# Kernel optimization log

Measured on AMD Instinct MI355X. Metric: run time of the kernel, lower is better.

Reference implementation:

```python
import jax, jax.numpy as jnp
import numpy as np

N = 1_000_000
C = 128
NBINS = 15


def setup_inputs() -> dict:
    key = jax.random.key(0)
    k1, k2 = jax.random.split(key)
    logits = jax.random.normal(k1, (N, C), dtype=jnp.float32)
    labels = jax.random.randint(k2, (N,), 0, C, dtype=jnp.int64)
    return {"logits": logits, "labels": labels}


def reference(logits, labels):
    n = logits.shape[0]
    probs = jax.nn.softmax(logits, axis=1)
    confidences = jnp.max(probs, axis=1)                      # [N]
    predictions = jnp.argmax(probs, axis=1)                   # [N]
    accuracies = (predictions == labels).astype(jnp.float32)  # [N]

    # Equal-count (adaptive) bin edges: interp(linspace(0,N,nbins+1), arange(N), sort(conf))
    sorted_conf = jnp.sort(confidences)
    q = jnp.linspace(0.0, float(n), NBINS + 1)
    edges = jnp.interp(q, jnp.arange(n, dtype=jnp.float32), sorted_conf)  # [NBINS+1]

    # Bin i covers (edges[i], edges[i+1]] to match conf.gt(lower) & conf.le(upper).
    idx = jnp.searchsorted(edges[1:-1], confidences, side="left")  # [N] in [0, NBINS-1]
    valid = (confidences > edges[0]) & (confidences <= edges[-1])
    idx = jnp.where(valid, idx, NBINS)  # dump out-of-range into extra segment

    cnt = jax.ops.segment_sum(jnp.ones_like(confidences), idx, num_segments=NBINS + 1)[:NBINS]
    csum = jax.ops.segment_sum(confidences, idx, num_segments=NBINS + 1)[:NBINS]
    asum = jax.ops.segment_sum(accuracies, idx, num_segments=NBINS + 1)[:NBINS]

    prop = cnt / jnp.float32(n)
    safe = jnp.maximum(cnt, 1.0)
    gap = jnp.abs(csum / safe - asum / safe)
    ece = jnp.sum(jnp.where(cnt > 0, gap * prop, 0.0))
    return ece.reshape(1)
```

## Files before the change

### kernel.cpp

```cpp
#include <hip/hip_runtime.h>
#include <hip/hip_bf16.h>
#include <cstdint>

#define NROWS 1000000
#define NCLS  128
#define NBINS 15

#define FBASE 0x3B000000u
#define NB    73728
#define SCAN_T 1024
#define PER   (NB / SCAN_T)

#define OFF_CONF   0u
#define OFF_ACC    4000000u
#define OFF_HIST   5000000u
#define OFF_SUB    5294912u
#define OFF_BINS   5417792u
#define OFF_DONE   5418152u
#define OFF_TGTB   5418168u
#define OFF_TGTL   5418288u
#define OFF_EDGES  5418408u
#define ZERO_BYTES (OFF_TGTB - OFF_HIST)

#define ROW_BLOCKS 2048

__device__ __forceinline__ void reduce_row(float4 v0, float4 v1, int l16,
                                           float& c_out, int& mi_out)
{
    const int b0 = l16 * 4, b1 = 64 + l16 * 4;
    float m = v0.x; int mi = b0;
    if (v0.y > m) { m = v0.y; mi = b0 + 1; }
    if (v0.z > m) { m = v0.z; mi = b0 + 2; }
    if (v0.w > m) { m = v0.w; mi = b0 + 3; }
    if (v1.x > m) { m = v1.x; mi = b1; }
    if (v1.y > m) { m = v1.y; mi = b1 + 1; }
    if (v1.z > m) { m = v1.z; mi = b1 + 2; }
    if (v1.w > m) { m = v1.w; mi = b1 + 3; }
#pragma unroll
    for (int d = 1; d < 16; d <<= 1) {
        float om = __shfl_xor(m, d);
        int   oi = __shfl_xor(mi, d);
        if (om > m || (om == m && oi < mi)) { m = om; mi = oi; }
    }
    float s = __expf(v0.x - m) + __expf(v0.y - m) + __expf(v0.z - m) + __expf(v0.w - m)
            + __expf(v1.x - m) + __expf(v1.y - m) + __expf(v1.z - m) + __expf(v1.w - m);
#pragma unroll
    for (int d = 1; d < 16; d <<= 1) s += __shfl_xor(s, d);
    c_out  = 1.0f / s;
    mi_out = mi;
}

__device__ __forceinline__ int bucket_of(float c)
{
    int ub = (int)(__float_as_uint(c) - FBASE);
    int b  = ub >> 10;
    return b < 0 ? 0 : (b >= NB ? NB - 1 : b);
}

__global__ __launch_bounds__(256) void k_row(const float* __restrict__ logits,
                                             const int* __restrict__ labels,
                                             float* __restrict__ conf,
                                             unsigned char* __restrict__ acc,
                                             unsigned int* __restrict__ hist)
{
    const int g   = threadIdx.x >> 4;
    const int l16 = threadIdx.x & 15;
    const float4* lg4 = reinterpret_cast<const float4*>(logits);

    for (long long base = (long long)blockIdx.x * 32; base < NROWS;
         base += (long long)ROW_BLOCKS * 32) {
        const long long rowA = base + g * 2;

        const float4* p = lg4 + rowA * (NCLS / 4) + l16;
        const float4 a0 = p[0],  a1 = p[16];
        const float4 b0 = p[32], b1 = p[48];
        const int2 lab = *reinterpret_cast<const int2*>(labels + rowA);

        float cA, cB; int miA, miB;
        reduce_row(a0, a1, l16, cA, miA);
        reduce_row(b0, b1, l16, cB, miB);

        if (l16 == 0) {
            *reinterpret_cast<float2*>(conf + rowA) = make_float2(cA, cB);
            uchar2 a;
            a.x = (lab.x == miA) ? 1 : 0;
            a.y = (lab.y == miB) ? 1 : 0;
            *reinterpret_cast<uchar2*>(acc + rowA) = a;
            atomicAdd(&hist[bucket_of(cA)], 1u);
            atomicAdd(&hist[bucket_of(cB)], 1u);
        }
    }
}

__device__ __forceinline__ unsigned int rank_of(int s)
{
    if (s == 0)  return 0u;
    if (s == 29) return (unsigned int)(NROWS - 1);
    int i = (s + 1) >> 1;
    unsigned int k = (unsigned int)((long long)i * NROWS / 15);
    return k + ((s & 1) ? 0u : 1u);
}

__global__ __launch_bounds__(SCAN_T) void k_scan(const unsigned int* __restrict__ hist,
                                                 int* __restrict__ tgtb,
                                                 int* __restrict__ tgtl)
{
    __shared__ unsigned int v[SCAN_T];
    const int t = threadIdx.x;
    unsigned int s = 0;
    for (int j = 0; j < PER; j++) s += hist[t * PER + j];
    v[t] = s;
    __syncthreads();
    for (int off = 1; off < SCAN_T; off <<= 1) {
        unsigned int x = (t >= off) ? v[t - off] : 0u;
        __syncthreads();
        v[t] += x;
        __syncthreads();
    }
    const unsigned int run0 = v[t] - s;
    for (int s2 = 0; s2 < 30; s2++) {
        unsigned int r = rank_of(s2);
        if (r >= run0 && r < run0 + s) {
            unsigned int run = run0;
            for (int j = 0; j < PER; j++) {
                unsigned int c = hist[t * PER + j];
                if (r < run + c) { tgtb[s2] = t * PER + j; tgtl[s2] = (int)(r - run); break; }
                run += c;
            }
        }
    }
}

__global__ __launch_bounds__(256) void k_subhist(const float* __restrict__ conf,
                                                 const int* __restrict__ tgtb,
                                                 const int* __restrict__ tgtl,
                                                 unsigned int* __restrict__ sub,
                                                 float* __restrict__ edges,
                                                 unsigned int* __restrict__ done)
{
    __shared__ int tb[30];
    if (threadIdx.x < 30) tb[threadIdx.x] = tgtb[threadIdx.x];
    __syncthreads();
    const int stride = gridDim.x * blockDim.x;
    for (int i = blockIdx.x * blockDim.x + threadIdx.x; i < NROWS / 4; i += stride) {
        float4 c4 = reinterpret_cast<const float4*>(conf)[i];
        float cv[4] = {c4.x, c4.y, c4.z, c4.w};
#pragma unroll
        for (int e = 0; e < 4; e++) {
            int ub = (int)(__float_as_uint(cv[e]) - FBASE);
            int b  = ub >> 10;
            b = b < 0 ? 0 : (b >= NB ? NB - 1 : b);
            int lo = ub & 1023;
            for (int s = 0; s < 30; s++)
                if (b == tb[s]) atomicAdd(&sub[s * 1024 + lo], 1u);
        }
    }

    __syncthreads();
    __shared__ unsigned int isLast;
    if (threadIdx.x == 0) {
        __threadfence();
        isLast = (atomicAdd(done, 1u) == gridDim.x - 1) ? 1u : 0u;
    }
    __syncthreads();
    if (!isLast) return;
    __threadfence();

    __shared__ float val[32];
    const int k = threadIdx.x & 31;
    for (int slot = threadIdx.x >> 5; slot < 30; slot += 8) {
        const unsigned int local = (unsigned int)tgtl[slot];
        unsigned int cs[32];
        unsigned int csum = 0;
        const unsigned int* q = sub + slot * 1024 + k * 32;
#pragma unroll
        for (int j = 0; j < 32; j++) { cs[j] = q[j]; csum += cs[j]; }
        unsigned int incl = csum;
#pragma unroll
        for (int off = 1; off < 32; off <<= 1) {
            unsigned int x = __shfl_up(incl, off);
            if (k >= off) incl += x;
        }
        const unsigned int excl = incl - csum;
        if (local >= excl && local < excl + csum) {
            unsigned int run = excl;
            int subidx = 0;
#pragma unroll
            for (int j = 0; j < 32; j++) {
                if (local >= run && local < run + cs[j]) subidx = k * 32 + j;
                run += cs[j];
            }
            unsigned int bits = FBASE + ((unsigned int)tb[slot] << 10) + (unsigned int)subidx;
            val[slot] = __uint_as_float(bits);
        }
    }
    __syncthreads();
    if (threadIdx.x == 0) {
        edges[0]  = val[0];
        edges[15] = val[29];
        for (int i = 1; i <= 14; i++) {
            double q = (double)i * (double)NROWS / 15.0;
            long long kk = (long long)i * NROWS / 15;
            double f = q - (double)kk;
            edges[i] = (float)((1.0 - f) * (double)val[2 * i - 1] + f * (double)val[2 * i]);
        }
    }
}

__global__ __launch_bounds__(256) void k_bin(const float* __restrict__ conf,
                                             const unsigned char* __restrict__ acc,
                                             const float* __restrict__ edges,
                                             double* __restrict__ bins,
                                             unsigned int* __restrict__ done,
                                             float* __restrict__ out)
{
    __shared__ float se[16];
    __shared__ float lc[4][16], ls[4][16], la[4][16];
    const int w = threadIdx.x >> 6;
    if (threadIdx.x < 16) se[threadIdx.x] = edges[threadIdx.x];
    if (threadIdx.x < 64) {
        int a = threadIdx.x >> 4, b = threadIdx.x & 15;
        lc[a][b] = 0.f; ls[a][b] = 0.f; la[a][b] = 0.f;
    }
    __syncthreads();
    const int stride = gridDim.x * blockDim.x;
    for (int i = blockIdx.x * blockDim.x + threadIdx.x; i < NROWS / 4; i += stride) {
        float4 c4 = reinterpret_cast<const float4*>(conf)[i];
        uchar4 a4 = reinterpret_cast<const uchar4*>(acc)[i];
        float cv[4] = {c4.x, c4.y, c4.z, c4.w};
        unsigned char av[4] = {a4.x, a4.y, a4.z, a4.w};
#pragma unroll
        for (int e = 0; e < 4; e++) {
            float v = cv[e];
            if (v > se[0] && v <= se[15]) {
                int idx = 0;
#pragma unroll
                for (int j = 1; j <= 14; j++) idx += (se[j] < v) ? 1 : 0;
                atomicAdd(&lc[w][idx], 1.0f);
                atomicAdd(&ls[w][idx], v);
                atomicAdd(&la[w][idx], (float)av[e]);
            }
        }
    }
    __syncthreads();
    if (threadIdx.x < 15) {
        int t = threadIdx.x;
        atomicAdd(&bins[t],      (double)(lc[0][t] + lc[1][t] + lc[2][t] + lc[3][t]));
        atomicAdd(&bins[15 + t], (double)(ls[0][t] + ls[1][t] + ls[2][t] + ls[3][t]));
        atomicAdd(&bins[30 + t], (double)(la[0][t] + la[1][t] + la[2][t] + la[3][t]));
    }

    __syncthreads();
    __shared__ unsigned int isLast;
    if (threadIdx.x == 0) {
        __threadfence();
        isLast = (atomicAdd(done, 1u) == gridDim.x - 1) ? 1u : 0u;
    }
    __syncthreads();
    if (isLast && threadIdx.x == 0) {
        __threadfence();
        double ece = 0.0;
        for (int b = 0; b < NBINS; b++) {
            double cnt = bins[b];
            if (cnt > 0.0) {
                double safe = cnt < 1.0 ? 1.0 : cnt;
                double gap  = fabs(bins[15 + b] / safe - bins[30 + b] / safe);
                ece += gap * (cnt / (double)NROWS);
            }
        }
        out[0] = (float)ece;
    }
}

extern "C" void kernel_launch(void* const* d_in, const int* in_sizes, int n_in,
                              void* d_out, int out_size, void* d_ws, size_t ws_size,
                              hipStream_t stream)
{
    const float* logits = (const float*)d_in[0];
    const int*   labels = (const int*)d_in[1];
    char* ws = (char*)d_ws;

    float*         conf  = (float*)(ws + OFF_CONF);
    unsigned char* acc   = (unsigned char*)(ws + OFF_ACC);
    unsigned int*  hist  = (unsigned int*)(ws + OFF_HIST);
    unsigned int*  sub   = (unsigned int*)(ws + OFF_SUB);
    double*        bins  = (double*)(ws + OFF_BINS);
    unsigned int*  done  = (unsigned int*)(ws + OFF_DONE);
    int*           tgtb  = (int*)(ws + OFF_TGTB);
    int*           tgtl  = (int*)(ws + OFF_TGTL);
    float*         edges = (float*)(ws + OFF_EDGES);

    hipMemsetAsync(ws + OFF_HIST, 0, ZERO_BYTES, stream);

    k_row<<<ROW_BLOCKS, 256, 0, stream>>>(logits, labels, conf, acc, hist);
    k_scan<<<1, SCAN_T, 0, stream>>>(hist, tgtb, tgtl);
    k_subhist<<<1024, 256, 0, stream>>>(conf, tgtb, tgtl, sub, edges, done);
    k_bin<<<1024, 256, 0, stream>>>(conf, acc, edges, bins, done + 1, (float*)d_out);
}
```

Baseline: 261.2 us.

## Streamline row softmax with swizzle reductions, ballot accuracy, transposed histogram

Rewrites the per-row kernel to launch one block per 32 rows, use ds_swizzle butterfly reductions, and compute confidence as exp(max)/sum(exp) without max subtraction. Accuracy is determined by checking whether the label's logit equals the row max via a ballot instead of tracking argmax. The bucket histogram is stored transposed so the scan kernel reads it coalesced, and the sub-histogram loop becomes a branch-free match followed by a single atomic. Dropping the max subtraction risks overflow for large logits, and the tie semantics of accuracy differ slightly from argmax.

Result: no change. 257.3 us (-1.5%).

```diff
diff --git a/kernel.cpp b/kernel.cpp
--- a/kernel.cpp
+++ b/kernel.cpp
@@ -22,72 +22,72 @@
 #define OFF_EDGES  5418408u
 #define ZERO_BYTES (OFF_TGTB - OFF_HIST)
 
-#define ROW_BLOCKS 2048
-
-__device__ __forceinline__ void reduce_row(float4 v0, float4 v1, int l16,
-                                           float& c_out, int& mi_out)
-{
-    const int b0 = l16 * 4, b1 = 64 + l16 * 4;
-    float m = v0.x; int mi = b0;
-    if (v0.y > m) { m = v0.y; mi = b0 + 1; }
-    if (v0.z > m) { m = v0.z; mi = b0 + 2; }
-    if (v0.w > m) { m = v0.w; mi = b0 + 3; }
-    if (v1.x > m) { m = v1.x; mi = b1; }
-    if (v1.y > m) { m = v1.y; mi = b1 + 1; }
-    if (v1.z > m) { m = v1.z; mi = b1 + 2; }
-    if (v1.w > m) { m = v1.w; mi = b1 + 3; }
-#pragma unroll
-    for (int d = 1; d < 16; d <<= 1) {
-        float om = __shfl_xor(m, d);
-        int   oi = __shfl_xor(mi, d);
-        if (om > m || (om == m && oi < mi)) { m = om; mi = oi; }
-    }
-    float s = __expf(v0.x - m) + __expf(v0.y - m) + __expf(v0.z - m) + __expf(v0.w - m)
-            + __expf(v1.x - m) + __expf(v1.y - m) + __expf(v1.z - m) + __expf(v1.w - m);
-#pragma unroll
-    for (int d = 1; d < 16; d <<= 1) s += __shfl_xor(s, d);
-    c_out  = 1.0f / s;
-    mi_out = mi;
-}
-
-__device__ __forceinline__ int bucket_of(float c)
-{
-    int ub = (int)(__float_as_uint(c) - FBASE);
-    int b  = ub >> 10;
-    return b < 0 ? 0 : (b >= NB ? NB - 1 : b);
+__device__ __forceinline__ float swz_max(float m, const int off)
+{
+    switch (off) {
+    case 1: return fmaxf(m, __uint_as_float(__builtin_amdgcn_ds_swizzle(__float_as_uint(m), 0x041F)));
+    case 2: return fmaxf(m, __uint_as_float(__builtin_amdgcn_ds_swizzle(__float_as_uint(m), 0x081F)));
+    case 4: return fmaxf(m, __uint_as_float(__builtin_amdgcn_ds_swizzle(__float_as_uint(m), 0x101F)));
+    default:return fmaxf(m, __uint_as_float(__builtin_amdgcn_ds_swizzle(__float_as_uint(m), 0x201F)));
+    }
+}
+__device__ __forceinline__ float swz_add(float s, const int off)
+{
+    switch (off) {
+    case 1: return s + __uint_as_float(__builtin_amdgcn_ds_swizzle(__float_as_uint(s), 0x041F));
+    case 2: return s + __uint_as_float(__builtin_amdgcn_ds_swizzle(__float_as_uint(s), 0x081F));
+    case 4: return s + __uint_as_float(__builtin_amdgcn_ds_swizzle(__float_as_uint(s), 0x101F));
+    default:return s + __uint_as_float(__builtin_amdgcn_ds_swizzle(__float_as_uint(s), 0x201F));
+    }
 }
 
 __global__ __launch_bounds__(256) void k_row(const float* __restrict__ logits,
                                              const int* __restrict__ labels,
                                              float* __restrict__ conf,
                                              unsigned char* __restrict__ acc,
-                                             unsigned int* __restrict__ hist)
-{
-    const int g   = threadIdx.x >> 4;
-    const int l16 = threadIdx.x & 15;
+                                             unsigned int* __restrict__ histT)
+{
+    const int lane = threadIdx.x & 63;
+    const int wv   = threadIdx.x >> 6;
+    const int g    = lane >> 4;
+    const int l16  = lane & 15;
+    const int wbase = blockIdx.x * 32 + wv * 8;
     const float4* lg4 = reinterpret_cast<const float4*>(logits);
 
-    for (long long base = (long long)blockIdx.x * 32; base < NROWS;
-         base += (long long)ROW_BLOCKS * 32) {
-        const long long rowA = base + g * 2;
-
-        const float4* p = lg4 + rowA * (NCLS / 4) + l16;
-        const float4 a0 = p[0],  a1 = p[16];
-        const float4 b0 = p[32], b1 = p[48];
-        const int2 lab = *reinterpret_cast<const int2*>(labels + rowA);
-
-        float cA, cB; int miA, miB;
-        reduce_row(a0, a1, l16, cA, miA);
-        reduce_row(b0, b1, l16, cB, miB);
-
-        if (l16 == 0) {
-            *reinterpret_cast<float2*>(conf + rowA) = make_float2(cA, cB);
-            uchar2 a;
-            a.x = (lab.x == miA) ? 1 : 0;
-            a.y = (lab.y == miB) ? 1 : 0;
-            *reinterpret_cast<uchar2*>(acc + rowA) = a;
-            atomicAdd(&hist[bucket_of(cA)], 1u);
-            atomicAdd(&hist[bucket_of(cB)], 1u);
+#pragma unroll
+    for (int half = 0; half < 2; half++) {
+        const int row = wbase + half * 4 + g;
+        const float4 v0 = lg4[row * 32 + l16];
+        const float4 v1 = lg4[row * 32 + 16 + l16];
+        const int lab = labels[row];
+
+        float m = fmaxf(fmaxf(fmaxf(v0.x, v0.y), fmaxf(v0.z, v0.w)),
+                        fmaxf(fmaxf(v1.x, v1.y), fmaxf(v1.z, v1.w)));
+        m = swz_max(m, 1); m = swz_max(m, 2); m = swz_max(m, 4); m = swz_max(m, 8);
+
+        float s = __expf(v0.x) + __expf(v0.y) + __expf(v0.z) + __expf(v0.w)
+                + __expf(v1.x) + __expf(v1.y) + __expf(v1.z) + __expf(v1.w);
+        s = swz_add(s, 1); s = swz_add(s, 2); s = swz_add(s, 4); s = swz_add(s, 8);
+
+        const float c = __expf(m) / s;
+
+        const bool hiHalf = (lab & 64) != 0;
+        const float cx = hiHalf ? v1.x : v0.x;
+        const float cy = hiHalf ? v1.y : v0.y;
+        const float cz = hiHalf ? v1.z : v0.z;
+        const float cw = hiHalf ? v1.w : v0.w;
+        const int e = lab & 3;
+        const float cand = (e == 0) ? cx : (e == 1) ? cy : (e == 2) ? cz : cw;
+        const bool hit = (((lab >> 2) & 15) == l16) && (cand == m);
+        const unsigned long long bal = __ballot(hit);
+
+        if (l16 == 15) {
+            conf[row] = c;
+            acc[row]  = ((bal >> (lane & 48)) & 0xFFFFull) ? 1u : 0u;
+            int ub = (int)(__float_as_uint(c) - FBASE);
+            int b  = ub >> 10;
+            b = b < 0 ? 0 : (b >= NB ? NB - 1 : b);
+            atomicAdd(&histT[(b % PER) * 1024 + b / PER], 1u);
         }
     }
 }
@@ -101,14 +101,14 @@
     return k + ((s & 1) ? 0u : 1u);
 }
 
-__global__ __launch_bounds__(SCAN_T) void k_scan(const unsigned int* __restrict__ hist,
+__global__ __launch_bounds__(SCAN_T) void k_scan(const unsigned int* __restrict__ histT,
                                                  int* __restrict__ tgtb,
                                                  int* __restrict__ tgtl)
 {
     __shared__ unsigned int v[SCAN_T];
     const int t = threadIdx.x;
     unsigned int s = 0;
-    for (int j = 0; j < PER; j++) s += hist[t * PER + j];
+    for (int j = 0; j < PER; j++) s += histT[j * 1024 + t];
     v[t] = s;
     __syncthreads();
     for (int off = 1; off < SCAN_T; off <<= 1) {
@@ -123,7 +123,7 @@
         if (r >= run0 && r < run0 + s) {
             unsigned int run = run0;
             for (int j = 0; j < PER; j++) {
-                unsigned int c = hist[t * PER + j];
+                unsigned int c = histT[j * 1024 + t];
                 if (r < run + c) { tgtb[s2] = t * PER + j; tgtl[s2] = (int)(r - run); break; }
                 run += c;
             }
@@ -151,8 +151,10 @@
             int b  = ub >> 10;
             b = b < 0 ? 0 : (b >= NB ? NB - 1 : b);
             int lo = ub & 1023;
-            for (int s = 0; s < 30; s++)
-                if (b == tb[s]) atomicAdd(&sub[s * 1024 + lo], 1u);
+            int match = -1;
+#pragma unroll
+            for (int s = 0; s < 30; s++) match = (b == tb[s]) ? s : match;
+            if (match >= 0) atomicAdd(&sub[match * 1024 + lo], 1u);
         }
     }
 
@@ -282,7 +284,7 @@
 
     float*         conf  = (float*)(ws + OFF_CONF);
     unsigned char* acc   = (unsigned char*)(ws + OFF_ACC);
-    unsigned int*  hist  = (unsigned int*)(ws + OFF_HIST);
+    unsigned int*  histT = (unsigned int*)(ws + OFF_HIST);
     unsigned int*  sub   = (unsigned int*)(ws + OFF_SUB);
     double*        bins  = (double*)(ws + OFF_BINS);
     unsigned int*  done  = (unsigned int*)(ws + OFF_DONE);
@@ -292,8 +294,8 @@
 
     hipMemsetAsync(ws + OFF_HIST, 0, ZERO_BYTES, stream);
 
-    k_row<<<ROW_BLOCKS, 256, 0, stream>>>(logits, labels, conf, acc, hist);
-    k_scan<<<1, SCAN_T, 0, stream>>>(hist, tgtb, tgtl);
+    k_row<<<NROWS / 32, 256, 0, stream>>>(logits, labels, conf, acc, histT);
+    k_scan<<<1, SCAN_T, 0, stream>>>(histT, tgtb, tgtl);
     k_subhist<<<1024, 256, 0, stream>>>(conf, tgtb, tgtl, sub, edges, done);
     k_bin<<<1024, 256, 0, stream>>>(conf, acc, edges, bins, done + 1, (float*)d_out);
 }
```
